# Kernel optimization log

Hardware: AMD Instinct MI355X
Metric: run time of the kernel (lower is better)

The kernel has to match this reference:

```python
import jax, jax.numpy as jnp
import numpy as np

N = 100000      # nodes
E = 800000      # edges
F_IN = 128      # input feature dim
HID = 32        # GAT out_channels per head
H = 4           # heads
HC = HID * H    # 128, concat width (== F_IN by design)
EDIM = 16       # raw edge feature dim
G = 256         # number of graphs in batch
OUT = 2         # output classes
SLOPE = 0.2     # GATConv LeakyReLU negative slope
BN_EPS = 1e-5


def setup_inputs() -> dict:
    key = jax.random.key(0)
    ks = jax.random.split(key, 16)
    s = 0.05
    x = jax.random.normal(ks[0], (N, F_IN), jnp.float32)
    edge_index = jax.random.randint(ks[1], (2, E), 0, N, dtype=jnp.int64)
    edge_attr = jax.random.normal(ks[2], (E, EDIM), jnp.float32)
    batch = jnp.sort(jax.random.randint(ks[3], (N,), 0, G, dtype=jnp.int64))
    edge_fc_W = jax.random.normal(ks[4], (EDIM, HID), jnp.float32) * s
    edge_fc_b = jnp.zeros((HID,), jnp.float32)
    # all 3 GAT layers have in_dim 128 -> H*C 128, so stack them
    Ws = jax.random.normal(ks[5], (3, F_IN, HC), jnp.float32) * s
    att_src = jax.random.normal(ks[6], (3, H, HID), jnp.float32) * s
    att_dst = jax.random.normal(ks[7], (3, H, HID), jnp.float32) * s
    att_edge = jax.random.normal(ks[8], (3, H, HID), jnp.float32) * s
    lin_e = jax.random.normal(ks[9], (3, HID, HC), jnp.float32) * s
    biases = jnp.zeros((3, HC), jnp.float32)
    bn_gamma = jnp.ones((3, HC), jnp.float32)
    bn_beta = jnp.zeros((3, HC), jnp.float32)
    fc_W = jax.random.normal(ks[10], (HC, OUT), jnp.float32) * s
    fc_b = jnp.zeros((OUT,), jnp.float32)
    return {"x": x, "edge_index": edge_index, "edge_attr": edge_attr, "batch": batch,
            "edge_fc_W": edge_fc_W, "edge_fc_b": edge_fc_b, "Ws": Ws,
            "att_src": att_src, "att_dst": att_dst, "att_edge": att_edge,
            "lin_e": lin_e, "biases": biases, "bn_gamma": bn_gamma,
            "bn_beta": bn_beta, "fc_W": fc_W, "fc_b": fc_b}


def _gat_layer(h, e_h, src, dst, W, a_s, a_d, a_e, We, b):
    xl = (h @ W).reshape(N, H, HID)            # [N,H,C]
    el = (e_h @ We).reshape(E, H, HID)         # [E,H,C]
    alpha = ((xl * a_s).sum(-1)[src]           # alpha_src gathered at source
             + (xl * a_d).sum(-1)[dst]         # alpha_dst gathered at target
             + (el * a_e).sum(-1))             # [E,H]
    alpha = jax.nn.leaky_relu(alpha, SLOPE)
    # segment softmax over incoming edges of each destination node
    amax = jax.ops.segment_max(alpha, dst, num_segments=N)
    ealpha = jnp.exp(alpha - amax[dst])
    denom = jax.ops.segment_sum(ealpha, dst, num_segments=N)
    alpha = ealpha / (denom[dst] + 1e-16)
    # weighted scatter-aggregate of source messages
    out = jax.ops.segment_sum(alpha[:, :, None] * xl[src], dst, num_segments=N)
    return out.reshape(N, HC) + b


def reference(x, edge_index, edge_attr, batch, edge_fc_W, edge_fc_b, Ws,
              att_src, att_dst, att_edge, lin_e, biases, bn_gamma, bn_beta,
              fc_W, fc_b):
    src, dst = edge_index[0], edge_index[1]
    e_h = edge_attr @ edge_fc_W + edge_fc_b   # [E, HID]
    h = x
    for l in range(3):
        h = _gat_layer(h, e_h, src, dst, Ws[l], att_src[l], att_dst[l],
                       att_edge[l], lin_e[l], biases[l])
        # BatchNorm1d over node dim (training-mode batch statistics)
        mu = h.mean(0)
        var = h.var(0)
        h = (h - mu) * jax.lax.rsqrt(var + BN_EPS) * bn_gamma[l] + bn_beta[l]
        h = jax.nn.relu(h)
        # dropout_rate = 0.0 -> identity
    # global mean pool per graph
    sums = jax.ops.segment_sum(h, batch, num_segments=G)
    cnt = jax.ops.segment_sum(jnp.ones((N,), h.dtype), batch, num_segments=G)
    pooled = sums / jnp.maximum(cnt, 1.0)[:, None]   # [G, HC]
    return pooled @ fc_W + fc_b                      # [G, OUT]
```

## Files before the change

### kernel.cpp

```cpp
#include <hip/hip_runtime.h>

#define Nn 100000
#define Ee 800000
#define HC 128
#define HID 32
#define NHD 4
#define EDIM 16
#define Gg 256
#define NOUT 2
#define SLOPE 0.2f
#define BN_EPS 1e-5f
#define SCHUNK 1024
#define NSB 98
#define NSLOT 64

typedef unsigned int u32;
typedef unsigned short u16;
typedef short v8s __attribute__((ext_vector_type(8)));
typedef float v4f __attribute__((ext_vector_type(4)));

union PkAB { u32 u[4]; v8s v; };

__device__ __forceinline__ float bflo(u32 u){ return __uint_as_float(u << 16); }
__device__ __forceinline__ float bfhi(u32 u){ return __uint_as_float(u & 0xFFFF0000u); }

__device__ __forceinline__ u32 bf16rne(float x)
{
  u32 b = __float_as_uint(x);
  return (b + 0x7FFFu + ((b >> 16) & 1u)) >> 16;
}
__device__ __forceinline__ u32 packsplit(float x)
{
  u32 hb = bf16rne(x);
  float hf = __uint_as_float(hb << 16);
  u32 lb = bf16rne(x - hf);
  return hb | (lb << 16);
}
__device__ __forceinline__ void split2(float f, u32& hb, u32& lb)
{
  hb = bf16rne(f);
  lb = bf16rne(f - __uint_as_float(hb << 16));
}

__global__ void compute_K(const float* __restrict__ efcW, const float* __restrict__ efcb,
                          const float* __restrict__ linE, const float* __restrict__ attE,
                          float* __restrict__ Kmat, float* __restrict__ kb)
{
  __shared__ float Msh[384];
  int t = threadIdx.x;
  if (t < 384) {
    int l = t >> 7, j = (t >> 2) & 31, h = t & 3;
    float m = 0.f;
    for (int c = 0; c < 32; ++c)
      m += linE[(l*32 + j)*128 + h*32 + c] * attE[(l*4 + h)*32 + c];
    Msh[l*128 + j*4 + h] = m;
  }
  __syncthreads();
  if (t < 192) {
    int k = t / 12, col = t % 12, l = col >> 2, h = col & 3;
    float acc = 0.f;
    for (int j = 0; j < 32; ++j)
      acc += efcW[k*32 + j] * Msh[l*128 + j*4 + h];
    Kmat[k*12 + col] = acc;
  } else if (t < 204) {
    int col = t - 192, l = col >> 2, h = col & 3;
    float acc = 0.f;
    for (int j = 0; j < 32; ++j)
      acc += efcb[j] * Msh[l*128 + j*4 + h];
    kb[col] = acc;
  }
}

__global__ void w_split(const float* __restrict__ Wall, u32* __restrict__ Wf)
{
  int tid = blockIdx.x * 256 + threadIdx.x;
  if (tid >= 3*HC*HC) return;
  int l = tid / (HC*HC);
  int rem = tid - l*HC*HC;
  int k = rem >> 7, n = rem & 127;
  u32 p = packsplit(Wall[tid]);
  int nt = n >> 4, col = n & 15;
  int ks = k >> 5, kin = k & 31, q = kin >> 3, j = kin & 7;
  int half = j >> 2, j4 = j & 3;
  int idx = ((((l*8 + nt)*4 + ks)*2 + half)*64 + q*16 + col)*4 + j4;
  Wf[idx] = p;
}

__global__ void k_hist(const int* __restrict__ dst, int* __restrict__ deg)
{
  int e = blockIdx.x * 256 + threadIdx.x;
  if (e < Ee) atomicAdd(&deg[dst[e]], 1);
}

__global__ void k_bsum(const int* __restrict__ deg, int* __restrict__ bsum)
{
  __shared__ int sh[256];
  int b = blockIdx.x, t = threadIdx.x;
  int s = 0;
  for (int i = t; i < SCHUNK; i += 256) {
    int idx = b*SCHUNK + i;
    if (idx < Nn) s += deg[idx];
  }
  sh[t] = s; __syncthreads();
  for (int o = 128; o; o >>= 1) { if (t < o) sh[t] += sh[t+o]; __syncthreads(); }
  if (!t) bsum[b] = sh[0];
}

__global__ void k_mid(const int* __restrict__ bsum, int* __restrict__ bpre, int* __restrict__ rowp)
{
  __shared__ int sh[NSB];
  int t = threadIdx.x;
  if (t < NSB) sh[t] = bsum[t];
  __syncthreads();
  if (!t) {
    int run = 0;
    for (int i = 0; i < NSB; ++i) { int v = sh[i]; sh[i] = run; run += v; }
    rowp[Nn] = run;
  }
  __syncthreads();
  if (t < NSB) bpre[t] = sh[t];
}

__global__ void k_scan(const int* __restrict__ deg, const int* __restrict__ bpre, int* __restrict__ rowp)
{
  __shared__ int sh[SCHUNK];
  int b = blockIdx.x, t = threadIdx.x;
  for (int i = t; i < SCHUNK; i += 256) {
    int idx = b*SCHUNK + i;
    sh[i] = (idx < Nn) ? deg[idx] : 0;
  }
  __syncthreads();
  if (!t) {
    int run = 0;
    for (int i = 0; i < SCHUNK; ++i) { int v = sh[i]; sh[i] = run; run += v; }
  }
  __syncthreads();
  int base = bpre[b];
  for (int i = t; i < SCHUNK; i += 256) {
    int idx = b*SCHUNK + i;
    if (idx < Nn) rowp[idx] = sh[i] + base;
  }
}

__global__ void k_fillpre(const int* __restrict__ src, const int* __restrict__ dst,
                          const float* __restrict__ eattr,
                          const float* __restrict__ Kmat, const float* __restrict__ kb,
                          const int* __restrict__ rowp, int* __restrict__ fill,
                          u32* __restrict__ rec)
{
  int e = blockIdx.x * 256 + threadIdx.x;
  if (e >= Ee) return;
  const float4* p = (const float4*)(eattr + (size_t)e * EDIM);
  float ea[16];
  #pragma unroll
  for (int qq = 0; qq < 4; ++qq) {
    float4 v = p[qq];
    ea[qq*4+0] = v.x; ea[qq*4+1] = v.y; ea[qq*4+2] = v.z; ea[qq*4+3] = v.w;
  }
  float ep[12];
  #pragma unroll
  for (int col = 0; col < 12; ++col) ep[col] = kb[col];
  #pragma unroll
  for (int k = 0; k < 16; ++k) {
    float v = ea[k];
    #pragma unroll
    for (int col = 0; col < 12; ++col) ep[col] += v * Kmat[k*12 + col];
  }
  int d = dst[e];
  int pos = rowp[d] + atomicAdd(&fill[d], 1);
  uint4 r0, r1;
  r0.x = bf16rne(ep[0])  | (bf16rne(ep[1])  << 16);
  r0.y = bf16rne(ep[2])  | (bf16rne(ep[3])  << 16);
  r0.z = bf16rne(ep[4])  | (bf16rne(ep[5])  << 16);
  r0.w = bf16rne(ep[6])  | (bf16rne(ep[7])  << 16);
  r1.x = bf16rne(ep[8])  | (bf16rne(ep[9])  << 16);
  r1.y = bf16rne(ep[10]) | (bf16rne(ep[11]) << 16);
  r1.z = (u32)src[e];
  r1.w = 0;
  uint4* rp = (uint4*)(rec + (size_t)pos * 8);
  rp[0] = r0; rp[1] = r1;
}

__device__ __forceinline__ int lbound(const int* __restrict__ a, int n, int key)
{
  int lo = 0, hi = n;
  while (lo < hi) {
    int mid = (lo + hi) >> 1;
    if (a[mid] < key) lo = mid + 1; else hi = mid;
  }
  return lo;
}

__global__ void k_gb(const int* __restrict__ batch, int* __restrict__ gb)
{
  int g = blockIdx.x * 256 + threadIdx.x;
  if (g <= Gg) gb[g] = lbound(batch, Nn, g);
}

__global__ void split_x(const float* __restrict__ src, u32* __restrict__ dst)
{
  int idx = blockIdx.x * 256 + threadIdx.x;
  if (idx >= Nn*HC/4) return;
  float4 v = ((const float4*)src)[idx];
  uint4 o;
  o.x = packsplit(v.x); o.y = packsplit(v.y);
  o.z = packsplit(v.z); o.w = packsplit(v.w);
  ((uint4*)dst)[idx] = o;
}

__global__ __launch_bounds__(256, 4) void gemm_mfma(const u32* __restrict__ Apk,
                                                    const u32* __restrict__ Wf,
                                                    u16* __restrict__ C2,
                                                    const float* __restrict__ aS,
                                                    const float* __restrict__ aD,
                                                    float* __restrict__ as_,
                                                    float* __restrict__ ad_,
                                                    const float* __restrict__ scb,
                                                    const float* __restrict__ shb,
                                                    int apply_bn)
{
  int t = threadIdx.x;
  int w = t >> 6, lane = t & 63;
  int col = lane & 15, q = lane >> 4;
  int rbase = blockIdx.x * 64 + w * 16;

  v4f acc[8];
  #pragma unroll
  for (int nt = 0; nt < 8; ++nt) acc[nt] = (v4f){0.f, 0.f, 0.f, 0.f};

  const uint4* Wf4 = (const uint4*)Wf;

  for (int ks = 0; ks < 4; ++ks) {
    PkAB Ah, Al;
    int ar = rbase + col;
    if (ar >= Nn) ar = Nn - 1;
    int cb = ks*32 + q*8;
    const uint4* pa = (const uint4*)(Apk + (size_t)ar*HC + cb);
    uint4 r0 = pa[0], r1 = pa[1];
    if (!apply_bn) {
      Ah.u[0] = (r0.x & 0xFFFFu) | (r0.y << 16);
      Al.u[0] = (r0.x >> 16)     | (r0.y & 0xFFFF0000u);
      Ah.u[1] = (r0.z & 0xFFFFu) | (r0.w << 16);
      Al.u[1] = (r0.z >> 16)     | (r0.w & 0xFFFF0000u);
      Ah.u[2] = (r1.x & 0xFFFFu) | (r1.y << 16);
      Al.u[2] = (r1.x >> 16)     | (r1.y & 0xFFFF0000u);
      Ah.u[3] = (r1.z & 0xFFFFu) | (r1.w << 16);
      Al.u[3] = (r1.z >> 16)     | (r1.w & 0xFFFF0000u);
    } else {
      float4 sc0 = *(const float4*)(scb + cb), sc1 = *(const float4*)(scb + cb + 4);
      float4 sh0 = *(const float4*)(shb + cb), sh1 = *(const float4*)(shb + cb + 4);
      float f0 = fmaxf((bflo(r0.x)+bfhi(r0.x))*sc0.x + sh0.x, 0.f);
      float f1 = fmaxf((bflo(r0.y)+bfhi(r0.y))*sc0.y + sh0.y, 0.f);
      float f2 = fmaxf((bflo(r0.z)+bfhi(r0.z))*sc0.z + sh0.z, 0.f);
      float f3 = fmaxf((bflo(r0.w)+bfhi(r0.w))*sc0.w + sh0.w, 0.f);
      float f4 = fmaxf((bflo(r1.x)+bfhi(r1.x))*sc1.x + sh1.x, 0.f);
      float f5 = fmaxf((bflo(r1.y)+bfhi(r1.y))*sc1.y + sh1.y, 0.f);
      float f6 = fmaxf((bflo(r1.z)+bfhi(r1.z))*sc1.z + sh1.z, 0.f);
      float f7 = fmaxf((bflo(r1.w)+bfhi(r1.w))*sc1.w + sh1.w, 0.f);
      u32 hb0,lb0,hb1,lb1,hb2,lb2,hb3,lb3,hb4,lb4,hb5,lb5,hb6,lb6,hb7,lb7;
      split2(f0,hb0,lb0); split2(f1,hb1,lb1); split2(f2,hb2,lb2); split2(f3,hb3,lb3);
      split2(f4,hb4,lb4); split2(f5,hb5,lb5); split2(f6,hb6,lb6); split2(f7,hb7,lb7);
      Ah.u[0] = hb0 | (hb1 << 16);  Al.u[0] = lb0 | (lb1 << 16);
      Ah.u[1] = hb2 | (hb3 << 16);  Al.u[1] = lb2 | (lb3 << 16);
      Ah.u[2] = hb4 | (hb5 << 16);  Al.u[2] = lb4 | (lb5 << 16);
      Ah.u[3] = hb6 | (hb7 << 16);  Al.u[3] = lb6 | (lb7 << 16);
    }
    #pragma unroll
    for (int nt = 0; nt < 8; ++nt) {
      uint4 b0 = Wf4[((nt*4 + ks)*2 + 0)*64 + lane];
      uint4 b1 = Wf4[((nt*4 + ks)*2 + 1)*64 + lane];
      PkAB Bh, Bl;
      Bh.u[0] = (b0.x & 0xFFFFu) | (b0.y << 16);
      Bl.u[0] = (b0.x >> 16)     | (b0.y & 0xFFFF0000u);
      Bh.u[1] = (b0.z & 0xFFFFu) | (b0.w << 16);
      Bl.u[1] = (b0.z >> 16)     | (b0.w & 0xFFFF0000u);
      Bh.u[2] = (b1.x & 0xFFFFu) | (b1.y << 16);
      Bl.u[2] = (b1.x >> 16)     | (b1.y & 0xFFFF0000u);
      Bh.u[3] = (b1.z & 0xFFFFu) | (b1.w << 16);
      Bl.u[3] = (b1.z >> 16)     | (b1.w & 0xFFFF0000u);
      acc[nt] = __builtin_amdgcn_mfma_f32_16x16x32_bf16(Ah.v, Bh.v, acc[nt], 0, 0, 0);
      acc[nt] = __builtin_amdgcn_mfma_f32_16x16x32_bf16(Ah.v, Bl.v, acc[nt], 0, 0, 0);
      acc[nt] = __builtin_amdgcn_mfma_f32_16x16x32_bf16(Al.v, Bh.v, acc[nt], 0, 0, 0);
    }
  }

  #pragma unroll
  for (int reg = 0; reg < 4; ++reg) {
    int row = rbase + q*4 + reg;
    if (row < Nn) {
      #pragma unroll
      for (int nt = 0; nt < 8; ++nt)
        C2[(size_t)row*HC + nt*16 + col] = (u16)bf16rne(acc[nt][reg]);
    }
  }

  #pragma unroll
  for (int h = 0; h < 4; ++h) {
    float a0 = aS[32*h + col], a1 = aS[32*h + 16 + col];
    float d0 = aD[32*h + col], d1 = aD[32*h + 16 + col];
    #pragma unroll
    for (int reg = 0; reg < 4; ++reg) {
      float s1 = acc[2*h][reg]*a0 + acc[2*h+1][reg]*a1;
      float s2 = acc[2*h][reg]*d0 + acc[2*h+1][reg]*d1;
      s1 += __shfl_xor(s1, 1); s1 += __shfl_xor(s1, 2);
      s1 += __shfl_xor(s1, 4); s1 += __shfl_xor(s1, 8);
      s2 += __shfl_xor(s2, 1); s2 += __shfl_xor(s2, 2);
      s2 += __shfl_xor(s2, 4); s2 += __shfl_xor(s2, 8);
      if (col == 0) {
        int row = rbase + q*4 + reg;
        if (row < Nn) {
          as_[row*NHD + h] = s1;
          ad_[row*NHD + h] = s2;
        }
      }
    }
  }
}

__global__ __launch_bounds__(256) void aggregate(const int* __restrict__ rowp, const u32* __restrict__ rec,
                                                 const float* __restrict__ as_, const float* __restrict__ ad_,
                                                 int l, const u32* __restrict__ xl2,
                                                 const float* __restrict__ bias, u32* __restrict__ outp,
                                                 float* __restrict__ psum, float* __restrict__ psq)
{
  __shared__ float4 rsum[256];
  __shared__ float4 rsq[256];
  int t = threadIdx.x;
  int n = blockIdx.x * 8 + (t >> 5);
  int c4 = t & 31;
  int h = c4 >> 3;
  float4 o = make_float4(0.f,0.f,0.f,0.f);
  bool valid = (n < Nn);
  if (valid) {
    int idx = l*4 + h;
    int p = idx >> 1, sel = idx & 1;
    float adh = ad_[n*NHD + h];
    int beg = rowp[n], end = rowp[n+1];
    float4 acc = make_float4(0.f,0.f,0.f,0.f);
    float wsum = 0.f;
    int i = beg;
    for (; i + 8 <= end; i += 8) {
      u32 eu[8]; int s[8]; float av[8]; uint2 v[8];
      #pragma unroll
      for (int j = 0; j < 8; ++j) eu[j] = rec[(size_t)(i+j)*8 + p];
      #pragma unroll
      for (int j = 0; j < 8; ++j) s[j] = (int)rec[(size_t)(i+j)*8 + 6];
      #pragma unroll
      for (int j = 0; j < 8; ++j) av[j] = as_[s[j]*NHD + h];
      #pragma unroll
      for (int j = 0; j < 8; ++j) v[j] = *(const uint2*)(xl2 + (size_t)s[j] * 64 + c4*2);
      #pragma unroll
      for (int j = 0; j < 8; ++j) {
        float ep = sel ? bfhi(eu[j]) : bflo(eu[j]);
        float a = ep + av[j] + adh;
        a = (a > 0.f) ? a : SLOPE * a;
        float wj = __expf(a);
        acc.x += wj*bflo(v[j].x); acc.y += wj*bfhi(v[j].x);
        acc.z += wj*bflo(v[j].y); acc.w += wj*bfhi(v[j].y);
        wsum += wj;
      }
    }
    for (; i < end; ++i) {
      u32 eu = rec[(size_t)i*8 + p];
      int s = (int)rec[(size_t)i*8 + 6];
      float ep = sel ? bfhi(eu) : bflo(eu);
      float a = ep + as_[s*NHD + h] + adh;
      a = (a > 0.f) ? a : SLOPE * a;
      float wj = __expf(a);
      uint2 v = *(const uint2*)(xl2 + (size_t)s * 64 + c4*2);
      acc.x += wj*bflo(v.x); acc.y += wj*bfhi(v.x);
      acc.z += wj*bflo(v.y); acc.w += wj*bfhi(v.y);
      wsum += wj;
    }
    float inv = 1.f / (wsum + 1e-16f);
    float4 b4 = *(const float4*)(bias + c4*4);
    o.x = acc.x*inv + b4.x; o.y = acc.y*inv + b4.y;
    o.z = acc.z*inv + b4.z; o.w = acc.w*inv + b4.w;
    uint4 w;
    w.x = packsplit(o.x); w.y = packsplit(o.y);
    w.z = packsplit(o.z); w.w = packsplit(o.w);
    *(uint4*)(outp + (size_t)n * HC + c4*4) = w;
  }
  rsum[t] = o;
  rsq[t] = make_float4(o.x*o.x, o.y*o.y, o.z*o.z, o.w*o.w);
  __syncthreads();
  for (int off = 128; off >= 32; off >>= 1) {
    if (t < off) {
      rsum[t].x += rsum[t+off].x; rsum[t].y += rsum[t+off].y;
      rsum[t].z += rsum[t+off].z; rsum[t].w += rsum[t+off].w;
      rsq[t].x  += rsq[t+off].x;  rsq[t].y  += rsq[t+off].y;
      rsq[t].z  += rsq[t+off].z;  rsq[t].w  += rsq[t+off].w;
    }
    __syncthreads();
  }
  if (t < 32) {
    int slot = blockIdx.x & (NSLOT-1);
    float4 s = rsum[t], q = rsq[t];
    atomicAdd(&psum[slot*HC + t*4+0], s.x);
    atomicAdd(&psum[slot*HC + t*4+1], s.y);
    atomicAdd(&psum[slot*HC + t*4+2], s.z);
    atomicAdd(&psum[slot*HC + t*4+3], s.w);
    atomicAdd(&psq[slot*HC + t*4+0], q.x);
    atomicAdd(&psq[slot*HC + t*4+1], q.y);
    atomicAdd(&psq[slot*HC + t*4+2], q.z);
    atomicAdd(&psq[slot*HC + t*4+3], q.w);
  }
}

__global__ void bn_final(float* __restrict__ psum, float* __restrict__ psq,
                         const float* __restrict__ gammaL, const float* __restrict__ betaL,
                         float* __restrict__ scb, float* __restrict__ shb)
{
  int c = threadIdx.x;
  float s = 0.f, q = 0.f;
  for (int k = 0; k < NSLOT; ++k) {
    s += psum[k*HC + c]; q += psq[k*HC + c];
    psum[k*HC + c] = 0.f; psq[k*HC + c] = 0.f;
  }
  float mu  = s * (1.f / Nn);
  float var = q * (1.f / Nn) - mu * mu;
  float sc = rsqrtf(var + BN_EPS) * gammaL[c];
  scb[c] = sc;
  shb[c] = betaL[c] - mu * sc;
}

__global__ __launch_bounds__(256) void pool2(const u32* __restrict__ Ap, const int* __restrict__ gb,
                                             const float* __restrict__ scb, const float* __restrict__ shb,
                                             float* __restrict__ pool)
{
  __shared__ float4 red[256];
  int g = blockIdx.x >> 2, qt = blockIdx.x & 3;
  int t = threadIdx.x;
  int cg = t & 7;
  int rs = t >> 3;
  int c4 = qt*8 + cg;
  int c = c4 * 4;
  int lo = gb[g], hi = gb[g+1];
  float4 s4 = *(const float4*)(scb + c);
  float4 t4 = *(const float4*)(shb + c);
  float4 acc = make_float4(0.f,0.f,0.f,0.f);
  for (int n = lo + rs; n < hi; n += 32) {
    uint4 v = *(const uint4*)(Ap + (size_t)n*HC + c);
    acc.x += fmaxf((bflo(v.x)+bfhi(v.x))*s4.x + t4.x, 0.f);
    acc.y += fmaxf((bflo(v.y)+bfhi(v.y))*s4.y + t4.y, 0.f);
    acc.z += fmaxf((bflo(v.z)+bfhi(v.z))*s4.z + t4.z, 0.f);
    acc.w += fmaxf((bflo(v.w)+bfhi(v.w))*s4.w + t4.w, 0.f);
  }
  red[t] = acc;
  __syncthreads();
  for (int off = 128; off >= 8; off >>= 1) {
    if (t < off) {
      red[t].x += red[t+off].x; red[t].y += red[t+off].y;
      red[t].z += red[t+off].z; red[t].w += red[t+off].w;
    }
    __syncthreads();
  }
  if (t < 8) {
    float inv = 1.f / fmaxf((float)(hi - lo), 1.f);
    float4 r = red[t];
    r.x *= inv; r.y *= inv; r.z *= inv; r.w *= inv;
    *(float4*)(pool + (size_t)g*HC + qt*32 + t*4) = r;
  }
}

__global__ void final_fc(const float* __restrict__ pool,
                         const float* __restrict__ fcW, const float* __restrict__ fcb,
                         float* __restrict__ out)
{
  int t = blockIdx.x * 256 + threadIdx.x;
  if (t >= Gg * NOUT) return;
  int g = t >> 1, o = t & 1;
  float acc = 0.f;
  for (int k = 0; k < HC; ++k)
    acc += pool[(size_t)g * HC + k] * fcW[k * NOUT + o];
  out[t] = acc + fcb[o];
}

extern "C" void kernel_launch(void* const* d_in, const int* in_sizes, int n_in,
                              void* d_out, int out_size, void* d_ws, size_t ws_size,
                              hipStream_t stream)
{
  const float* x      = (const float*)d_in[0];
  const int*   eidx   = (const int*)d_in[1];
  const float* eattr  = (const float*)d_in[2];
  const int*   batch  = (const int*)d_in[3];
  const float* efcW   = (const float*)d_in[4];
  const float* efcb   = (const float*)d_in[5];
  const float* Wall   = (const float*)d_in[6];
  const float* attS   = (const float*)d_in[7];
  const float* attD   = (const float*)d_in[8];
  const float* attE   = (const float*)d_in[9];
  const float* linE   = (const float*)d_in[10];
  const float* biases = (const float*)d_in[11];
  const float* gamma  = (const float*)d_in[12];
  const float* beta   = (const float*)d_in[13];
  const float* fcW    = (const float*)d_in[14];
  const float* fcb    = (const float*)d_in[15];
  float* out = (float*)d_out;

  const int* src = eidx;
  const int* dst = eidx + Ee;

  float* ws    = (float*)d_ws;
  float* bufA  = ws;
  float* bufB  = bufA + (size_t)Nn*HC;
  float* as_   = bufB + (size_t)Nn*HC;
  float* ad_   = as_ + (size_t)Nn*NHD;
  float* Kmat  = ad_ + (size_t)Nn*NHD;
  float* kb    = Kmat + 192;
  float* scb   = kb + 16;
  float* shb   = scb + 128;
  float* pool  = shb + 128;
  u32*   rec   = (u32*)(pool + (size_t)Gg*HC);
  u32*   Wf    = rec + (size_t)Ee*8;
  float* psum  = (float*)(Wf + 3*HC*HC);
  float* psq   = psum + NSLOT*HC;
  int*   gb    = (int*)(psq + NSLOT*HC);
  int*   rowp  = gb + (Gg + 3);
  int*   deg   = rowp + (Nn + 1);
  int*   fill  = deg + Nn;
  int*   bsum  = fill + Nn;
  int*   bpre  = bsum + 128;

  w_split<<<(3*HC*HC + 255)/256, 256, 0, stream>>>(Wall, Wf);
  compute_K<<<1, 512, 0, stream>>>(efcW, efcb, linE, attE, Kmat, kb);
  k_gb<<<2, 256, 0, stream>>>(batch, gb);

  hipMemsetAsync(deg, 0, 2*Nn*sizeof(int), stream);
  hipMemsetAsync(psum, 0, 2*NSLOT*HC*sizeof(float), stream);
  k_hist<<<(Ee + 255)/256, 256, 0, stream>>>(dst, deg);
  k_bsum<<<NSB, 256, 0, stream>>>(deg, bsum);
  k_mid<<<1, 128, 0, stream>>>(bsum, bpre, rowp);
  k_scan<<<NSB, 256, 0, stream>>>(deg, bpre, rowp);
  k_fillpre<<<(Ee + 255)/256, 256, 0, stream>>>(src, dst, eattr, Kmat, kb, rowp, fill, rec);

  split_x<<<(Nn*HC/4 + 255)/256, 256, 0, stream>>>(x, (u32*)bufA);

  for (int l = 0; l < 3; ++l) {
    gemm_mfma<<<(Nn + 63)/64, 256, 0, stream>>>((const u32*)bufA, Wf + (size_t)l*HC*HC, (u16*)bufB,
                                                attS + l*HC, attD + l*HC, as_, ad_,
                                                scb, shb, (l > 0) ? 1 : 0);
    aggregate<<<(Nn + 7)/8, 256, 0, stream>>>(rowp, rec, as_, ad_, l, (const u32*)bufB,
                                              biases + l*HC, (u32*)bufA, psum, psq);
    bn_final<<<1, 128, 0, stream>>>(psum, psq, gamma + l*HC, beta + l*HC, scb, shb);
  }

  pool2<<<Gg*4, 256, 0, stream>>>((const u32*)bufA, gb, scb, shb, pool);
  final_fc<<<2, 256, 0, stream>>>(pool, fcW, fcb, out);
}
```

Baseline: 716.2 us.

## Widen aggregate to 8 channels per thread and replace BN atomics with per-block partials

The aggregate kernel now gives each thread 8 channels with 16-byte gathers and covers 16 nodes per block. This halves the redundant per-edge index and attention loads and doubles gather width. BatchNorm statistics are now written as per-block partials and reduced by a new two-stage kernel, replacing the contended atomic slots. The GEMM also preloads all A-tile rows into registers before the k-loop. The changes add an extra launch and about 6.4 MB of partial-sum traffic per layer, and halve the number of threads available per node.

```diff
diff --git a/kernel.cpp b/kernel.cpp
--- a/kernel.cpp
+++ b/kernel.cpp
@@ -12,7 +12,7 @@
 #define BN_EPS 1e-5f
 #define SCHUNK 1024
 #define NSB 98
-#define NSLOT 64
+#define NBAG 6250
 
 typedef unsigned int u32;
 typedef unsigned short u16;
@@ -230,13 +230,21 @@
 
   const uint4* Wf4 = (const uint4*)Wf;
 
+  int ar = rbase + col;
+  if (ar >= Nn) ar = Nn - 1;
+  const uint4* pa = (const uint4*)(Apk + (size_t)ar*HC);
+  uint4 ra[8];
+  #pragma unroll
+  for (int ks = 0; ks < 4; ++ks) {
+    ra[2*ks]   = pa[ks*8 + q*2];
+    ra[2*ks+1] = pa[ks*8 + q*2 + 1];
+  }
+
+  #pragma unroll
   for (int ks = 0; ks < 4; ++ks) {
     PkAB Ah, Al;
-    int ar = rbase + col;
-    if (ar >= Nn) ar = Nn - 1;
     int cb = ks*32 + q*8;
-    const uint4* pa = (const uint4*)(Apk + (size_t)ar*HC + cb);
-    uint4 r0 = pa[0], r1 = pa[1];
+    uint4 r0 = ra[2*ks], r1 = ra[2*ks+1];
     if (!apply_bn) {
       Ah.u[0] = (r0.x & 0xFFFFu) | (r0.y << 16);
       Al.u[0] = (r0.x >> 16)     | (r0.y & 0xFFFF0000u);
@@ -323,24 +331,26 @@
                                                  const float* __restrict__ bias, u32* __restrict__ outp,
                                                  float* __restrict__ psum, float* __restrict__ psq)
 {
-  __shared__ float4 rsum[256];
-  __shared__ float4 rsq[256];
+  __shared__ float4 rsA[256], rsB[256], rqA[256], rqB[256];
   int t = threadIdx.x;
-  int n = blockIdx.x * 8 + (t >> 5);
-  int c4 = t & 31;
-  int h = c4 >> 3;
-  float4 o = make_float4(0.f,0.f,0.f,0.f);
-  bool valid = (n < Nn);
-  if (valid) {
+  int n = blockIdx.x * 16 + (t >> 4);
+  int c8 = t & 15;
+  int h = c8 >> 2;
+  float o[8];
+  #pragma unroll
+  for (int k = 0; k < 8; ++k) o[k] = 0.f;
+  if (n < Nn) {
     int idx = l*4 + h;
     int p = idx >> 1, sel = idx & 1;
     float adh = ad_[n*NHD + h];
     int beg = rowp[n], end = rowp[n+1];
-    float4 acc = make_float4(0.f,0.f,0.f,0.f);
+    float acc[8];
+    #pragma unroll
+    for (int k = 0; k < 8; ++k) acc[k] = 0.f;
     float wsum = 0.f;
     int i = beg;
     for (; i + 8 <= end; i += 8) {
-      u32 eu[8]; int s[8]; float av[8]; uint2 v[8];
+      u32 eu[8]; int s[8]; float av[8]; uint4 v[8];
       #pragma unroll
       for (int j = 0; j < 8; ++j) eu[j] = rec[(size_t)(i+j)*8 + p];
       #pragma unroll
@@ -348,15 +358,17 @@
       #pragma unroll
       for (int j = 0; j < 8; ++j) av[j] = as_[s[j]*NHD + h];
       #pragma unroll
-      for (int j = 0; j < 8; ++j) v[j] = *(const uint2*)(xl2 + (size_t)s[j] * 64 + c4*2);
+      for (int j = 0; j < 8; ++j) v[j] = *(const uint4*)(xl2 + (size_t)s[j] * 64 + c8*4);
       #pragma unroll
       for (int j = 0; j < 8; ++j) {
         float ep = sel ? bfhi(eu[j]) : bflo(eu[j]);
         float a = ep + av[j] + adh;
         a = (a > 0.f) ? a : SLOPE * a;
         float wj = __expf(a);
-        acc.x += wj*bflo(v[j].x); acc.y += wj*bfhi(v[j].x);
-        acc.z += wj*bflo(v[j].y); acc.w += wj*bfhi(v[j].y);
+        acc[0] += wj*bflo(v[j].x); acc[1] += wj*bfhi(v[j].x);
+        acc[2] += wj*bflo(v[j].y); acc[3] += wj*bfhi(v[j].y);
+        acc[4] += wj*bflo(v[j].z); acc[5] += wj*bfhi(v[j].z);
+        acc[6] += wj*bflo(v[j].w); acc[7] += wj*bfhi(v[j].w);
         wsum += wj;
       }
     }
@@ -367,61 +379,94 @@
       float a = ep + as_[s*NHD + h] + adh;
       a = (a > 0.f) ? a : SLOPE * a;
       float wj = __expf(a);
-      uint2 v = *(const uint2*)(xl2 + (size_t)s * 64 + c4*2);
-      acc.x += wj*bflo(v.x); acc.y += wj*bfhi(v.x);
-      acc.z += wj*bflo(v.y); acc.w += wj*bfhi(v.y);
+      uint4 v = *(const uint4*)(xl2 + (size_t)s * 64 + c8*4);
+      acc[0] += wj*bflo(v.x); acc[1] += wj*bfhi(v.x);
+      acc[2] += wj*bflo(v.y); acc[3] += wj*bfhi(v.y);
+      acc[4] += wj*bflo(v.z); acc[5] += wj*bfhi(v.z);
+      acc[6] += wj*bflo(v.w); acc[7] += wj*bfhi(v.w);
       wsum += wj;
     }
     float inv = 1.f / (wsum + 1e-16f);
-    float4 b4 = *(const float4*)(bias + c4*4);
-    o.x = acc.x*inv + b4.x; o.y = acc.y*inv + b4.y;
-    o.z = acc.z*inv + b4.z; o.w = acc.w*inv + b4.w;
-    uint4 w;
-    w.x = packsplit(o.x); w.y = packsplit(o.y);
-    w.z = packsplit(o.z); w.w = packsplit(o.w);
-    *(uint4*)(outp + (size_t)n * HC + c4*4) = w;
-  }
-  rsum[t] = o;
-  rsq[t] = make_float4(o.x*o.x, o.y*o.y, o.z*o.z, o.w*o.w);
+    uint4 w0, w1;
+    #pragma unroll
+    for (int k = 0; k < 8; ++k) o[k] = acc[k]*inv + bias[c8*8 + k];
+    w0.x = packsplit(o[0]); w0.y = packsplit(o[1]);
+    w0.z = packsplit(o[2]); w0.w = packsplit(o[3]);
+    w1.x = packsplit(o[4]); w1.y = packsplit(o[5]);
+    w1.z = packsplit(o[6]); w1.w = packsplit(o[7]);
+    uint4* op = (uint4*)(outp + (size_t)n * HC + c8*8);
+    op[0] = w0; op[1] = w1;
+  }
+  rsA[t] = make_float4(o[0], o[1], o[2], o[3]);
+  rsB[t] = make_float4(o[4], o[5], o[6], o[7]);
+  rqA[t] = make_float4(o[0]*o[0], o[1]*o[1], o[2]*o[2], o[3]*o[3]);
+  rqB[t] = make_float4(o[4]*o[4], o[5]*o[5], o[6]*o[6], o[7]*o[7]);
+  __syncthreads();
+  for (int off = 128; off >= 16; off >>= 1) {
+    if (t < off) {
+      rsA[t].x += rsA[t+off].x; rsA[t].y += rsA[t+off].y;
+      rsA[t].z += rsA[t+off].z; rsA[t].w += rsA[t+off].w;
+      rsB[t].x += rsB[t+off].x; rsB[t].y += rsB[t+off].y;
+      rsB[t].z += rsB[t+off].z; rsB[t].w += rsB[t+off].w;
+      rqA[t].x += rqA[t+off].x; rqA[t].y += rqA[t+off].y;
+      rqA[t].z += rqA[t+off].z; rqA[t].w += rqA[t+off].w;
+      rqB[t].x += rqB[t+off].x; rqB[t].y += rqB[t+off].y;
+      rqB[t].z += rqB[t+off].z; rqB[t].w += rqB[t+off].w;
+    }
+    __syncthreads();
+  }
+  if (t < 16) {
+    float4* ps = (float4*)(psum + (size_t)blockIdx.x*HC + t*8);
+    ps[0] = rsA[t]; ps[1] = rsB[t];
+    float4* pq = (float4*)(psq + (size_t)blockIdx.x*HC + t*8);
+    pq[0] = rqA[t]; pq[1] = rqB[t];
+  }
+}
+
+__global__ __launch_bounds__(256) void k_bnpart(const float* __restrict__ psum, const float* __restrict__ psq,
+                                                float* __restrict__ gsum, float* __restrict__ gsq)
+{
+  __shared__ float4 rs[256], rq[256];
+  int t = threadIdx.x;
+  int c4 = t & 31, rg = t >> 5;
+  float4 s = make_float4(0.f,0.f,0.f,0.f), q = make_float4(0.f,0.f,0.f,0.f);
+  for (int k = blockIdx.x*8 + rg; k < NBAG; k += 64*8) {
+    float4 a = *(const float4*)(psum + (size_t)k*HC + c4*4);
+    float4 b = *(const float4*)(psq  + (size_t)k*HC + c4*4);
+    s.x += a.x; s.y += a.y; s.z += a.z; s.w += a.w;
+    q.x += b.x; q.y += b.y; q.z += b.z; q.w += b.w;
+  }
+  rs[t] = s; rq[t] = q;
   __syncthreads();
   for (int off = 128; off >= 32; off >>= 1) {
     if (t < off) {
-      rsum[t].x += rsum[t+off].x; rsum[t].y += rsum[t+off].y;
-      rsum[t].z += rsum[t+off].z; rsum[t].w += rsum[t+off].w;
-      rsq[t].x  += rsq[t+off].x;  rsq[t].y  += rsq[t+off].y;
-      rsq[t].z  += rsq[t+off].z;  rsq[t].w  += rsq[t+off].w;
+      rs[t].x += rs[t+off].x; rs[t].y += rs[t+off].y;
+      rs[t].z += rs[t+off].z; rs[t].w += rs[t+off].w;
+      rq[t].x += rq[t+off].x; rq[t].y += rq[t+off].y;
+      rq[t].z += rq[t+off].z; rq[t].w += rq[t+off].w;
     }
     __syncthreads();
   }
   if (t < 32) {
-    int slot = blockIdx.x & (NSLOT-1);
-    float4 s = rsum[t], q = rsq[t];
-    atomicAdd(&psum[slot*HC + t*4+0], s.x);
-    atomicAdd(&psum[slot*HC + t*4+1], s.y);
-    atomicAdd(&psum[slot*HC + t*4+2], s.z);
-    atomicAdd(&psum[slot*HC + t*4+3], s.w);
-    atomicAdd(&psq[slot*HC + t*4+0], q.x);
-    atomicAdd(&psq[slot*HC + t*4+1], q.y);
-    atomicAdd(&psq[slot*HC + t*4+2], q.z);
-    atomicAdd(&psq[slot*HC + t*4+3], q.w);
-  }
-}
-
-__global__ void bn_final(float* __restrict__ psum, float* __restrict__ psq,
-                         const float* __restrict__ gammaL, const float* __restrict__ betaL,
-                         float* __restrict__ scb, float* __restrict__ shb)
+    atomicAdd(&gsum[t*4+0], rs[t].x); atomicAdd(&gsum[t*4+1], rs[t].y);
+    atomicAdd(&gsum[t*4+2], rs[t].z); atomicAdd(&gsum[t*4+3], rs[t].w);
+    atomicAdd(&gsq[t*4+0], rq[t].x);  atomicAdd(&gsq[t*4+1], rq[t].y);
+    atomicAdd(&gsq[t*4+2], rq[t].z);  atomicAdd(&gsq[t*4+3], rq[t].w);
+  }
+}
+
+__global__ void k_bnfin(float* __restrict__ gsum, float* __restrict__ gsq,
+                        const float* __restrict__ gammaL, const float* __restrict__ betaL,
+                        float* __restrict__ scb, float* __restrict__ shb)
 {
   int c = threadIdx.x;
-  float s = 0.f, q = 0.f;
-  for (int k = 0; k < NSLOT; ++k) {
-    s += psum[k*HC + c]; q += psq[k*HC + c];
-    psum[k*HC + c] = 0.f; psq[k*HC + c] = 0.f;
-  }
+  float s = gsum[c], q = gsq[c];
   float mu  = s * (1.f / Nn);
   float var = q * (1.f / Nn) - mu * mu;
   float sc = rsqrtf(var + BN_EPS) * gammaL[c];
   scb[c] = sc;
   shb[c] = betaL[c] - mu * sc;
+  gsum[c] = 0.f; gsq[c] = 0.f;
 }
 
 __global__ __launch_bounds__(256) void pool2(const u32* __restrict__ Ap, const int* __restrict__ gb,
@@ -510,12 +555,14 @@
   float* kb    = Kmat + 192;
   float* scb   = kb + 16;
   float* shb   = scb + 128;
-  float* pool  = shb + 128;
+  float* gsum  = shb + 128;
+  float* gsq   = gsum + 128;
+  float* pool  = gsq + 128;
   u32*   rec   = (u32*)(pool + (size_t)Gg*HC);
   u32*   Wf    = rec + (size_t)Ee*8;
   float* psum  = (float*)(Wf + 3*HC*HC);
-  float* psq   = psum + NSLOT*HC;
-  int*   gb    = (int*)(psq + NSLOT*HC);
+  float* psq   = psum + (size_t)NBAG*HC;
+  int*   gb    = (int*)(psq + (size_t)NBAG*HC);
   int*   rowp  = gb + (Gg + 3);
   int*   deg   = rowp + (Nn + 1);
   int*   fill  = deg + Nn;
@@ -527,7 +574,7 @@
   k_gb<<<2, 256, 0, stream>>>(batch, gb);
 
   hipMemsetAsync(deg, 0, 2*Nn*sizeof(int), stream);
-  hipMemsetAsync(psum, 0, 2*NSLOT*HC*sizeof(float), stream);
+  hipMemsetAsync(gsum, 0, 256*sizeof(float), stream);
   k_hist<<<(Ee + 255)/256, 256, 0, stream>>>(dst, deg);
   k_bsum<<<NSB, 256, 0, stream>>>(deg, bsum);
   k_mid<<<1, 128, 0, stream>>>(bsum, bpre, rowp);
@@ -540,9 +587,10 @@
     gemm_mfma<<<(Nn + 63)/64, 256, 0, stream>>>((const u32*)bufA, Wf + (size_t)l*HC*HC, (u16*)bufB,
                                                 attS + l*HC, attD + l*HC, as_, ad_,
                                                 scb, shb, (l > 0) ? 1 : 0);
-    aggregate<<<(Nn + 7)/8, 256, 0, stream>>>(rowp, rec, as_, ad_, l, (const u32*)bufB,
-                                              biases + l*HC, (u32*)bufA, psum, psq);
-    bn_final<<<1, 128, 0, stream>>>(psum, psq, gamma + l*HC, beta + l*HC, scb, shb);
+    aggregate<<<NBAG, 256, 0, stream>>>(rowp, rec, as_, ad_, l, (const u32*)bufB,
+                                        biases + l*HC, (u32*)bufA, psum, psq);
+    k_bnpart<<<64, 256, 0, stream>>>(psum, psq, gsum, gsq);
+    k_bnfin<<<1, 128, 0, stream>>>(gsum, gsq, gamma + l*HC, beta + l*HC, scb, shb);
   }
 
   pool2<<<Gg*4, 256, 0, stream>>>((const u32*)bufA, gb, scb, shb, pool);
```

Result: faster. 647.8 us (-9.6%).
